# Performance work log

Measured on AMD Instinct MI355X. Metric: run time of the kernel, lower is better.

Reference implementation:

```python
import jax, jax.numpy as jnp
import numpy as np

B, T, C, H = 2, 2048, 1024, 16
HD = C // H  # 64

def setup_inputs() -> dict:
    key = jax.random.key(0)
    ks = jax.random.split(key, 9)
    s = 0.02
    return {
        "x": jax.random.normal(ks[0], (B, T, C), jnp.float32),
        "Wq": jax.random.normal(ks[1], (C, C), jnp.float32) * s,
        "bq": jax.random.normal(ks[2], (C,), jnp.float32) * s,
        "Wk": jax.random.normal(ks[3], (C, C), jnp.float32) * s,
        "bk": jax.random.normal(ks[4], (C,), jnp.float32) * s,
        "Wv": jax.random.normal(ks[5], (C, C), jnp.float32) * s,
        "bv": jax.random.normal(ks[6], (C,), jnp.float32) * s,
        "Wp": jax.random.normal(ks[7], (C, C), jnp.float32) * s,
        "bp": jax.random.normal(ks[8], (C,), jnp.float32) * s,
    }

def reference(x, Wq, bq, Wk, bk, Wv, bv, Wp, bp):
    Bb, Tt, Cc = x.shape
    hd = Cc // H
    # project and split heads: [B, H, T, hd]
    def heads(W, b):
        return (x @ W.T + b).reshape(Bb, Tt, H, hd).transpose(0, 2, 1, 3)
    q, k, v = heads(Wq, bq), heads(Wk, bk), heads(Wv, bv)
    scale = 1.0 / np.sqrt(hd).astype(np.float32)
    att = jnp.einsum('bhqd,bhkd->bhqk', q, k) * scale
    causal = jnp.tril(jnp.ones((Tt, Tt), bool))
    att = jnp.where(causal[None, None], att, -jnp.inf)
    att = jax.nn.softmax(att, axis=-1)
    y = jnp.einsum('bhqk,bhkd->bhqd', att, v)
    y = y.transpose(0, 2, 1, 3).reshape(Bb, Tt, Cc)
    return y @ Wp.T + bp
```

## Files before the change

kernel.cpp:

```cpp
#include <hip/hip_runtime.h>
#include <hip/hip_bf16.h>

#define Tsz 2048
#define Csz 1024
#define Hn 16

typedef short s8v __attribute__((ext_vector_type(8)));
typedef short s4v __attribute__((ext_vector_type(4)));
typedef float f4v __attribute__((ext_vector_type(4)));

#define QSCALE (0.125f * 1.44269504088896f)

__device__ __forceinline__ short bf_bits(float x) {
    __hip_bfloat16 t = __float2bfloat16(x);
    return *reinterpret_cast<short*>(&t);
}

__device__ __forceinline__ void gload_lds(const void* g, void* l) {
    __builtin_amdgcn_global_load_lds(
        (const __attribute__((address_space(1))) void*)g,
        (__attribute__((address_space(3))) void*)l, 16, 0, 0);
}

__global__ void cvt6(const float* __restrict__ x, const float* __restrict__ wq,
                     const float* __restrict__ wk, const float* __restrict__ wv,
                     const float* __restrict__ wp,
                     short* __restrict__ xo, short* __restrict__ qo,
                     short* __restrict__ ko, short* __restrict__ vo,
                     short* __restrict__ po) {
    const int bx = blockIdx.x;
    const float* in; short* out; int ib;
    if (bx < 4096) { in = x; out = xo; ib = bx; }
    else {
        const int r = bx - 4096, w = r >> 10;
        ib = r & 1023;
        switch (w) {
            case 0: in = wq; out = qo; break;
            case 1: in = wk; out = ko; break;
            case 2: in = wv; out = vo; break;
            default: in = wp; out = po; break;
        }
    }
    const int i = ib * 1024 + threadIdx.x * 4;
    float4 v = *(const float4*)(in + i);
    short4 o;
    o.x = bf_bits(v.x); o.y = bf_bits(v.y); o.z = bf_bits(v.z); o.w = bf_bits(v.w);
    *(short4*)(out + i) = o;
}

__global__ __launch_bounds__(256, 3) void qkv_gemm(
    const short* __restrict__ X,
    const short* __restrict__ Wq, const short* __restrict__ Wk, const short* __restrict__ Wv,
    const float* __restrict__ bq, const float* __restrict__ bk, const float* __restrict__ bv,
    short* __restrict__ Qo, short* __restrict__ Ko, short* __restrict__ Vto)
{
    const int z = blockIdx.z;
    const short* W = (z == 0) ? Wq : (z == 1) ? Wk : Wv;
    const float* bias = (z == 0) ? bq : (z == 1) ? bk : bv;

    __shared__ __align__(16) short Ash[128 * 32];
    __shared__ __align__(16) short Bsh[128 * 32];
    __shared__ __align__(16) short TR[64 * 72];

    const int tid = threadIdx.x, lane = tid & 63, wave = tid >> 6;
    const int ln = lane & 15, hi = lane >> 4;
    const int m0 = blockIdx.x * 128, n0 = blockIdx.y * 128;
    const int wm = (wave >> 1) * 64, wn = (wave & 1) * 64;

    const short* Ag = X + (size_t)(m0 + (tid >> 2)) * Csz + (tid & 3) * 8;
    const short* Bg = W + (size_t)(n0 + (tid >> 2)) * Csz + (tid & 3) * 8;

    f4v acc[4][4];
    #pragma unroll
    for (int mt = 0; mt < 4; mt++)
        #pragma unroll
        for (int nt = 0; nt < 4; nt++)
            #pragma unroll
            for (int i = 0; i < 4; i++) acc[mt][nt][i] = 0.f;

    for (int k0 = 0; k0 < Csz; k0 += 32) {
        __syncthreads();
        gload_lds(Ag + k0, Ash + tid * 8);
        gload_lds(Ag + k0 + (size_t)64 * Csz, Ash + 2048 + tid * 8);
        gload_lds(Bg + k0, Bsh + tid * 8);
        gload_lds(Bg + k0 + (size_t)64 * Csz, Bsh + 2048 + tid * 8);
        __syncthreads();

        s8v af[4], bfr[4];
        #pragma unroll
        for (int mt = 0; mt < 4; mt++)
            af[mt] = *(const s8v*)(Ash + (wm + mt * 16 + ln) * 32 + hi * 8);
        #pragma unroll
        for (int nt = 0; nt < 4; nt++)
            bfr[nt] = *(const s8v*)(Bsh + (wn + nt * 16 + ln) * 32 + hi * 8);
        #pragma unroll
        for (int mt = 0; mt < 4; mt++)
            #pragma unroll
            for (int nt = 0; nt < 4; nt++)
                acc[mt][nt] = __builtin_amdgcn_mfma_f32_16x16x32_bf16(af[mt], bfr[nt], acc[mt][nt], 0, 0, 0);
    }

    if (z == 2) {
        const int b = m0 >> 11, t0 = m0 & 2047;
        float bvv[4];
        #pragma unroll
        for (int nt = 0; nt < 4; nt++) bvv[nt] = bias[n0 + wn + nt * 16 + ln];
        #pragma unroll
        for (int ph = 0; ph < 4; ph++) {
            const int mh = ph >> 1, nh = ph & 1;
            __syncthreads();
            if ((wave >> 1) == mh && (wave & 1) == nh) {
                #pragma unroll
                for (int mt = 0; mt < 4; mt++)
                    #pragma unroll
                    for (int nt = 0; nt < 4; nt++) {
                        s4v pk;
                        #pragma unroll
                        for (int i = 0; i < 4; i++) pk[i] = bf_bits(acc[mt][nt][i] + bvv[nt]);
                        *(s4v*)(TR + (nt * 16 + ln) * 72 + mt * 16 + hi * 4) = pk;
                    }
            }
            __syncthreads();
            const int chl = tid >> 2, seg = tid & 3;
            const s8v r0 = *(const s8v*)(TR + chl * 72 + seg * 16);
            const s8v r1 = *(const s8v*)(TR + chl * 72 + seg * 16 + 8);
            short* dst = Vto + (size_t)(b * 1024 + n0 + nh * 64 + chl) * Tsz + t0 + mh * 64 + seg * 16;
            *(s8v*)(dst) = r0;
            *(s8v*)(dst + 8) = r1;
        }
        return;
    }

    const float scale = (z == 0) ? QSCALE : 1.0f;
    short* out = (z == 0) ? Qo : Ko;

    #pragma unroll
    for (int nt = 0; nt < 4; nt++) {
        const int col = n0 + wn + nt * 16 + ln;
        const float bvv = bias[col];
        #pragma unroll
        for (int mt = 0; mt < 4; mt++) {
            const int row0 = m0 + wm + mt * 16 + hi * 4;
            #pragma unroll
            for (int i = 0; i < 4; i++)
                out[(size_t)(row0 + i) * Csz + col] = bf_bits((acc[mt][nt][i] + bvv) * scale);
        }
    }
}

__global__ __launch_bounds__(256, 2) void proj_gemm(
    const short* __restrict__ A, const short* __restrict__ W,
    const float* __restrict__ bias, float* __restrict__ out)
{
    __shared__ __align__(16) short Ash[128 * 32];
    __shared__ __align__(16) short Bsh[128 * 32];

    const int tid = threadIdx.x, lane = tid & 63, wave = tid >> 6;
    const int ln = lane & 15, hi = lane >> 4;
    const int m0 = blockIdx.x * 128, n0 = blockIdx.y * 128;
    const int wm = (wave >> 1) * 64, wn = (wave & 1) * 64;

    const short* Ag = A + (size_t)(m0 + (tid >> 2)) * Csz + (tid & 3) * 8;
    const short* Bg = W + (size_t)(n0 + (tid >> 2)) * Csz + (tid & 3) * 8;

    f4v acc[4][4];
    #pragma unroll
    for (int mt = 0; mt < 4; mt++)
        #pragma unroll
        for (int nt = 0; nt < 4; nt++)
            #pragma unroll
            for (int i = 0; i < 4; i++) acc[mt][nt][i] = 0.f;

    for (int k0 = 0; k0 < Csz; k0 += 32) {
        __syncthreads();
        gload_lds(Ag + k0, Ash + tid * 8);
        gload_lds(Ag + k0 + (size_t)64 * Csz, Ash + 2048 + tid * 8);
        gload_lds(Bg + k0, Bsh + tid * 8);
        gload_lds(Bg + k0 + (size_t)64 * Csz, Bsh + 2048 + tid * 8);
        __syncthreads();

        s8v af[4], bfr[4];
        #pragma unroll
        for (int mt = 0; mt < 4; mt++)
            af[mt] = *(const s8v*)(Ash + (wm + mt * 16 + ln) * 32 + hi * 8);
        #pragma unroll
        for (int nt = 0; nt < 4; nt++)
            bfr[nt] = *(const s8v*)(Bsh + (wn + nt * 16 + ln) * 32 + hi * 8);
        #pragma unroll
        for (int mt = 0; mt < 4; mt++)
            #pragma unroll
            for (int nt = 0; nt < 4; nt++)
                acc[mt][nt] = __builtin_amdgcn_mfma_f32_16x16x32_bf16(af[mt], bfr[nt], acc[mt][nt], 0, 0, 0);
    }

    #pragma unroll
    for (int nt = 0; nt < 4; nt++) {
        const int col = n0 + wn + nt * 16 + ln;
        const float bvv = bias[col];
        #pragma unroll
        for (int mt = 0; mt < 4; mt++)
            #pragma unroll
            for (int i = 0; i < 4; i++)
                out[(size_t)(m0 + wm + mt * 16 + hi * 4 + i) * Csz + col] = acc[mt][nt][i] + bvv;
    }
}

__global__ __launch_bounds__(512, 2) void attn7(
    const short* __restrict__ Q, const short* __restrict__ Kg,
    const short* __restrict__ Vt, short* __restrict__ Y)
{
    __shared__ __align__(16) short Ksh[2][64 * 72];
    __shared__ __align__(16) short Vsh[2][64 * 72];
    __shared__ __align__(16) short Psh[8][16 * 72];

    const int tid = threadIdx.x, lane = tid & 63, wave = tid >> 6;
    const int wv = wave & 3, g = wave >> 2;
    const int ln = lane & 15, hi = lane >> 4;
    const int p = blockIdx.x;
    const int qts[2] = { g ? 15 - p : p, g ? 16 + p : 31 - p };
    const int bh = blockIdx.y;
    const size_t base = (size_t)(bh >> 4) * Tsz * Csz + (size_t)(bh & 15) * 64;
    const size_t vtbase = (size_t)bh * 64 * Tsz;
    const int qrel = wv * 16 + ln;
    short* Pq = Psh[wave];

    s8v qf[2][2];
    #pragma unroll
    for (int t = 0; t < 2; t++)
        #pragma unroll
        for (int kk = 0; kk < 2; kk++)
            qf[t][kk] = *(const s8v*)(Q + base + (size_t)(qts[t] * 64 + qrel) * Csz + kk * 32 + hi * 8);

    f4v o[2][4];
    float lsum[2] = {0.f, 0.f};
    #pragma unroll
    for (int t = 0; t < 2; t++)
        #pragma unroll
        for (int dt = 0; dt < 4; dt++)
            #pragma unroll
            for (int i = 0; i < 4; i++) o[t][dt][i] = 0.f;

    const int sr = tid >> 3, sc = (tid & 7) * 8;
    const short* Kp = Kg + base + (size_t)sr * Csz + sc;
    const short* Vp = Vt + vtbase + (size_t)sr * Tsz + sc;
    const int swo = sr * 72 + sc;

    const int nkb = 32 - p;

    s8v kR = *(const s8v*)(Kp);
    s8v vR = *(const s8v*)(Vp);
    *(s8v*)(&Ksh[0][swo]) = kR;
    *(s8v*)(&Vsh[0][swo]) = vR;
    kR = *(const s8v*)(Kp + (size_t)64 * Csz);
    vR = *(const s8v*)(Vp + 64);
    __syncthreads();

    for (int kb = 0; kb < nkb; kb++) {
        const int buf = kb & 1;
        if (kb + 1 < nkb) {
            *(s8v*)(&Ksh[buf ^ 1][swo]) = kR;
            *(s8v*)(&Vsh[buf ^ 1][swo]) = vR;
            const int knx = (kb + 2 < nkb) ? (kb + 2) * 64 : (nkb - 1) * 64;
            kR = *(const s8v*)(Kp + (size_t)knx * Csz);
            vR = *(const s8v*)(Vp + knx);
        }

        s8v kf[2][4], vf[2][4];
        #pragma unroll
        for (int nt = 0; nt < 4; nt++)
            #pragma unroll
            for (int kk = 0; kk < 2; kk++) {
                kf[kk][nt] = *(const s8v*)(&Ksh[buf][(nt * 16 + ln) * 72 + kk * 32 + hi * 8]);
                vf[kk][nt] = *(const s8v*)(&Vsh[buf][(nt * 16 + ln) * 72 + kk * 32 + hi * 8]);
            }

        #pragma unroll
        for (int t = 0; t < 2; t++) {
            if (kb > qts[t]) continue;
            const bool dg = (kb == qts[t]);

            f4v s[4];
            #pragma unroll
            for (int nt = 0; nt < 4; nt++) {
                #pragma unroll
                for (int i = 0; i < 4; i++) s[nt][i] = 0.f;
                s[nt] = __builtin_amdgcn_mfma_f32_16x16x32_bf16(kf[0][nt], qf[t][0], s[nt], 0, 0, 0);
                s[nt] = __builtin_amdgcn_mfma_f32_16x16x32_bf16(kf[1][nt], qf[t][1], s[nt], 0, 0, 0);
            }

            #pragma unroll
            for (int nt = 0; nt < 4; nt++) {
                float pv[4];
                #pragma unroll
                for (int i = 0; i < 4; i++) pv[i] = exp2f(s[nt][i]);
                if (dg) {
                    const int kr = nt * 16 + hi * 4;
                    #pragma unroll
                    for (int i = 0; i < 4; i++)
                        if (kr + i > qrel) pv[i] = 0.f;
                }
                lsum[t] += (pv[0] + pv[1]) + (pv[2] + pv[3]);
                s4v w;
                #pragma unroll
                for (int i = 0; i < 4; i++) w[i] = bf_bits(pv[i]);
                *(s4v*)(Pq + ln * 72 + nt * 16 + hi * 4) = w;
            }
            const s8v pb0 = *(const s8v*)(Pq + ln * 72 + hi * 8);
            const s8v pb1 = *(const s8v*)(Pq + ln * 72 + 32 + hi * 8);

            #pragma unroll
            for (int dt = 0; dt < 4; dt++) {
                o[t][dt] = __builtin_amdgcn_mfma_f32_16x16x32_bf16(vf[0][dt], pb0, o[t][dt], 0, 0, 0);
                o[t][dt] = __builtin_amdgcn_mfma_f32_16x16x32_bf16(vf[1][dt], pb1, o[t][dt], 0, 0, 0);
            }
        }
        __syncthreads();
    }

    #pragma unroll
    for (int t = 0; t < 2; t++) {
        float l = lsum[t];
        l += __shfl_xor(l, 16);
        l += __shfl_xor(l, 32);
        const float inv = 1.0f / l;
        const int qrow = qts[t] * 64 + qrel;
        #pragma unroll
        for (int dt = 0; dt < 4; dt++) {
            s4v w;
            #pragma unroll
            for (int i = 0; i < 4; i++) w[i] = bf_bits(o[t][dt][i] * inv);
            *(s4v*)(Y + base + (size_t)qrow * Csz + dt * 16 + hi * 4) = w;
        }
    }
}

extern "C" void kernel_launch(void* const* d_in, const int* in_sizes, int n_in,
                              void* d_out, int out_size, void* d_ws, size_t ws_size,
                              hipStream_t stream) {
    const float* x  = (const float*)d_in[0];
    const float* Wq = (const float*)d_in[1];
    const float* bq = (const float*)d_in[2];
    const float* Wk = (const float*)d_in[3];
    const float* bk = (const float*)d_in[4];
    const float* Wv = (const float*)d_in[5];
    const float* bv = (const float*)d_in[6];
    const float* Wp = (const float*)d_in[7];
    const float* bp = (const float*)d_in[8];

    char* ws = (char*)d_ws;
    short* Xb  = (short*)(ws);
    short* Wqb = (short*)(ws + (8u  << 20));
    short* Wkb = (short*)(ws + (10u << 20));
    short* Wvb = (short*)(ws + (12u << 20));
    short* Wpb = (short*)(ws + (14u << 20));
    short* Qb  = (short*)(ws + (16u << 20));
    short* Kb  = (short*)(ws + (24u << 20));
    short* Vtb = (short*)(ws + (32u << 20));
    short* Yb  = (short*)(ws + (40u << 20));

    hipLaunchKernelGGL(cvt6, dim3(8192), dim3(256), 0, stream,
                       x, Wq, Wk, Wv, Wp, Xb, Wqb, Wkb, Wvb, Wpb);

    hipLaunchKernelGGL(qkv_gemm, dim3(32, 8, 3), dim3(256), 0, stream,
                       Xb, Wqb, Wkb, Wvb, bq, bk, bv, Qb, Kb, Vtb);

    hipLaunchKernelGGL(attn7, dim3(8, 32), dim3(512), 0, stream, Qb, Kb, Vtb, Yb);

    hipLaunchKernelGGL(proj_gemm, dim3(32, 8), dim3(256), 0, stream, Yb, Wpb, bp, (float*)d_out);
}
```

Baseline: 191.4 us.

## Split attention into 256-thread blocks with 32 query rows per wave

Rewrites the attention kernel so each 256-thread block processes a balanced pair of query tiles, with each wave computing 32 query rows against shared K/V tiles. The grid doubles to 512 blocks to improve CU fill, and per-wave work per LDS fragment load increases. Waves whose query tile is finished skip fragment loads. In exchange, K/V tiles are reloaded by twice as many blocks, and the QKV GEMM occupancy hint is lowered to give it more registers.

```diff
diff --git a/kernel.cpp b/kernel.cpp
--- a/kernel.cpp
+++ b/kernel.cpp
@@ -48,7 +48,7 @@
     *(short4*)(out + i) = o;
 }
 
-__global__ __launch_bounds__(256, 3) void qkv_gemm(
+__global__ __launch_bounds__(256, 2) void qkv_gemm(
     const short* __restrict__ X,
     const short* __restrict__ Wq, const short* __restrict__ Wk, const short* __restrict__ Wv,
     const float* __restrict__ bq, const float* __restrict__ bk, const float* __restrict__ bv,
@@ -205,130 +205,146 @@
     }
 }
 
-__global__ __launch_bounds__(512, 2) void attn7(
+__global__ __launch_bounds__(256, 2) void attn8(
     const short* __restrict__ Q, const short* __restrict__ Kg,
     const short* __restrict__ Vt, short* __restrict__ Y)
 {
     __shared__ __align__(16) short Ksh[2][64 * 72];
     __shared__ __align__(16) short Vsh[2][64 * 72];
-    __shared__ __align__(16) short Psh[8][16 * 72];
+    __shared__ __align__(16) short Psh[4][32 * 72];
 
     const int tid = threadIdx.x, lane = tid & 63, wave = tid >> 6;
-    const int wv = wave & 3, g = wave >> 2;
     const int ln = lane & 15, hi = lane >> 4;
     const int p = blockIdx.x;
-    const int qts[2] = { g ? 15 - p : p, g ? 16 + p : 31 - p };
+    const int qt = (wave >> 1) ? (31 - p) : p;
+    const int qh = wave & 1;
+    const int q0 = qt * 64 + qh * 32;
     const int bh = blockIdx.y;
     const size_t base = (size_t)(bh >> 4) * Tsz * Csz + (size_t)(bh & 15) * 64;
     const size_t vtbase = (size_t)bh * 64 * Tsz;
-    const int qrel = wv * 16 + ln;
     short* Pq = Psh[wave];
 
     s8v qf[2][2];
     #pragma unroll
-    for (int t = 0; t < 2; t++)
+    for (int j = 0; j < 2; j++)
         #pragma unroll
         for (int kk = 0; kk < 2; kk++)
-            qf[t][kk] = *(const s8v*)(Q + base + (size_t)(qts[t] * 64 + qrel) * Csz + kk * 32 + hi * 8);
+            qf[j][kk] = *(const s8v*)(Q + base + (size_t)(q0 + j * 16 + ln) * Csz + kk * 32 + hi * 8);
 
     f4v o[2][4];
     float lsum[2] = {0.f, 0.f};
     #pragma unroll
-    for (int t = 0; t < 2; t++)
+    for (int j = 0; j < 2; j++)
         #pragma unroll
         for (int dt = 0; dt < 4; dt++)
             #pragma unroll
-            for (int i = 0; i < 4; i++) o[t][dt][i] = 0.f;
-
-    const int sr = tid >> 3, sc = (tid & 7) * 8;
+            for (int i = 0; i < 4; i++) o[j][dt][i] = 0.f;
+
+    const int sr = tid >> 2, sc = (tid & 3) * 16;
     const short* Kp = Kg + base + (size_t)sr * Csz + sc;
     const short* Vp = Vt + vtbase + (size_t)sr * Tsz + sc;
     const int swo = sr * 72 + sc;
 
     const int nkb = 32 - p;
 
-    s8v kR = *(const s8v*)(Kp);
-    s8v vR = *(const s8v*)(Vp);
-    *(s8v*)(&Ksh[0][swo]) = kR;
-    *(s8v*)(&Vsh[0][swo]) = vR;
-    kR = *(const s8v*)(Kp + (size_t)64 * Csz);
-    vR = *(const s8v*)(Vp + 64);
+    s8v kR0 = *(const s8v*)(Kp);
+    s8v kR1 = *(const s8v*)(Kp + 8);
+    s8v vR0 = *(const s8v*)(Vp);
+    s8v vR1 = *(const s8v*)(Vp + 8);
+    *(s8v*)(&Ksh[0][swo]) = kR0; *(s8v*)(&Ksh[0][swo + 8]) = kR1;
+    *(s8v*)(&Vsh[0][swo]) = vR0; *(s8v*)(&Vsh[0][swo + 8]) = vR1;
+    kR0 = *(const s8v*)(Kp + (size_t)64 * Csz);
+    kR1 = *(const s8v*)(Kp + (size_t)64 * Csz + 8);
+    vR0 = *(const s8v*)(Vp + 64);
+    vR1 = *(const s8v*)(Vp + 64 + 8);
     __syncthreads();
 
     for (int kb = 0; kb < nkb; kb++) {
         const int buf = kb & 1;
         if (kb + 1 < nkb) {
-            *(s8v*)(&Ksh[buf ^ 1][swo]) = kR;
-            *(s8v*)(&Vsh[buf ^ 1][swo]) = vR;
+            *(s8v*)(&Ksh[buf ^ 1][swo]) = kR0; *(s8v*)(&Ksh[buf ^ 1][swo + 8]) = kR1;
+            *(s8v*)(&Vsh[buf ^ 1][swo]) = vR0; *(s8v*)(&Vsh[buf ^ 1][swo + 8]) = vR1;
             const int knx = (kb + 2 < nkb) ? (kb + 2) * 64 : (nkb - 1) * 64;
-            kR = *(const s8v*)(Kp + (size_t)knx * Csz);
-            vR = *(const s8v*)(Vp + knx);
-        }
-
-        s8v kf[2][4], vf[2][4];
-        #pragma unroll
-        for (int nt = 0; nt < 4; nt++)
-            #pragma unroll
-            for (int kk = 0; kk < 2; kk++) {
-                kf[kk][nt] = *(const s8v*)(&Ksh[buf][(nt * 16 + ln) * 72 + kk * 32 + hi * 8]);
-                vf[kk][nt] = *(const s8v*)(&Vsh[buf][(nt * 16 + ln) * 72 + kk * 32 + hi * 8]);
-            }
-
-        #pragma unroll
-        for (int t = 0; t < 2; t++) {
-            if (kb > qts[t]) continue;
-            const bool dg = (kb == qts[t]);
-
-            f4v s[4];
-            #pragma unroll
-            for (int nt = 0; nt < 4; nt++) {
-                #pragma unroll
-                for (int i = 0; i < 4; i++) s[nt][i] = 0.f;
-                s[nt] = __builtin_amdgcn_mfma_f32_16x16x32_bf16(kf[0][nt], qf[t][0], s[nt], 0, 0, 0);
-                s[nt] = __builtin_amdgcn_mfma_f32_16x16x32_bf16(kf[1][nt], qf[t][1], s[nt], 0, 0, 0);
-            }
-
-            #pragma unroll
-            for (int nt = 0; nt < 4; nt++) {
-                float pv[4];
-                #pragma unroll
-                for (int i = 0; i < 4; i++) pv[i] = exp2f(s[nt][i]);
-                if (dg) {
-                    const int kr = nt * 16 + hi * 4;
+            kR0 = *(const s8v*)(Kp + (size_t)knx * Csz);
+            kR1 = *(const s8v*)(Kp + (size_t)knx * Csz + 8);
+            vR0 = *(const s8v*)(Vp + knx);
+            vR1 = *(const s8v*)(Vp + knx + 8);
+        }
+
+        if (kb <= qt) {
+            s8v kf[2][4], vf[2][4];
+            #pragma unroll
+            for (int nt = 0; nt < 4; nt++)
+                #pragma unroll
+                for (int kk = 0; kk < 2; kk++) {
+                    kf[kk][nt] = *(const s8v*)(&Ksh[buf][(nt * 16 + ln) * 72 + kk * 32 + hi * 8]);
+                    vf[kk][nt] = *(const s8v*)(&Vsh[buf][(nt * 16 + ln) * 72 + kk * 32 + hi * 8]);
+                }
+
+            const bool dg = (kb == qt);
+
+            f4v s[4][2];
+            #pragma unroll
+            for (int nt = 0; nt < 4; nt++)
+                #pragma unroll
+                for (int j = 0; j < 2; j++) {
                     #pragma unroll
-                    for (int i = 0; i < 4; i++)
-                        if (kr + i > qrel) pv[i] = 0.f;
+                    for (int i = 0; i < 4; i++) s[nt][j][i] = 0.f;
+                    s[nt][j] = __builtin_amdgcn_mfma_f32_16x16x32_bf16(kf[0][nt], qf[j][0], s[nt][j], 0, 0, 0);
+                    s[nt][j] = __builtin_amdgcn_mfma_f32_16x16x32_bf16(kf[1][nt], qf[j][1], s[nt][j], 0, 0, 0);
                 }
-                lsum[t] += (pv[0] + pv[1]) + (pv[2] + pv[3]);
-                s4v w;
-                #pragma unroll
-                for (int i = 0; i < 4; i++) w[i] = bf_bits(pv[i]);
-                *(s4v*)(Pq + ln * 72 + nt * 16 + hi * 4) = w;
-            }
-            const s8v pb0 = *(const s8v*)(Pq + ln * 72 + hi * 8);
-            const s8v pb1 = *(const s8v*)(Pq + ln * 72 + 32 + hi * 8);
-
-            #pragma unroll
-            for (int dt = 0; dt < 4; dt++) {
-                o[t][dt] = __builtin_amdgcn_mfma_f32_16x16x32_bf16(vf[0][dt], pb0, o[t][dt], 0, 0, 0);
-                o[t][dt] = __builtin_amdgcn_mfma_f32_16x16x32_bf16(vf[1][dt], pb1, o[t][dt], 0, 0, 0);
-            }
-        }
-        __syncthreads();
-    }
-
-    #pragma unroll
-    for (int t = 0; t < 2; t++) {
-        float l = lsum[t];
+
+            #pragma unroll
+            for (int nt = 0; nt < 4; nt++)
+                #pragma unroll
+                for (int j = 0; j < 2; j++) {
+                    float pv[4];
+                    #pragma unroll
+                    for (int i = 0; i < 4; i++) pv[i] = exp2f(s[nt][j][i]);
+                    if (dg) {
+                        const int kr = nt * 16 + hi * 4;
+                        const int qr = qh * 32 + j * 16 + ln;
+                        #pragma unroll
+                        for (int i = 0; i < 4; i++)
+                            if (kr + i > qr) pv[i] = 0.f;
+                    }
+                    lsum[j] += (pv[0] + pv[1]) + (pv[2] + pv[3]);
+                    s4v w;
+                    #pragma unroll
+                    for (int i = 0; i < 4; i++) w[i] = bf_bits(pv[i]);
+                    *(s4v*)(Pq + (j * 16 + ln) * 72 + nt * 16 + hi * 4) = w;
+                }
+
+            s8v pb[2][2];
+            #pragma unroll
+            for (int j = 0; j < 2; j++)
+                #pragma unroll
+                for (int kk = 0; kk < 2; kk++)
+                    pb[j][kk] = *(const s8v*)(Pq + (j * 16 + ln) * 72 + kk * 32 + hi * 8);
+
+            #pragma unroll
+            for (int dt = 0; dt < 4; dt++)
+                #pragma unroll
+                for (int j = 0; j < 2; j++) {
+                    o[j][dt] = __builtin_amdgcn_mfma_f32_16x16x32_bf16(vf[0][dt], pb[j][0], o[j][dt], 0, 0, 0);
+                    o[j][dt] = __builtin_amdgcn_mfma_f32_16x16x32_bf16(vf[1][dt], pb[j][1], o[j][dt], 0, 0, 0);
+                }
+        }
+        __syncthreads();
+    }
+
+    #pragma unroll
+    for (int j = 0; j < 2; j++) {
+        float l = lsum[j];
         l += __shfl_xor(l, 16);
         l += __shfl_xor(l, 32);
         const float inv = 1.0f / l;
-        const int qrow = qts[t] * 64 + qrel;
+        const int qrow = q0 + j * 16 + ln;
         #pragma unroll
         for (int dt = 0; dt < 4; dt++) {
             s4v w;
             #pragma unroll
-            for (int i = 0; i < 4; i++) w[i] = bf_bits(o[t][dt][i] * inv);
+            for (int i = 0; i < 4; i++) w[i] = bf_bits(o[j][dt][i] * inv);
             *(s4v*)(Y + base + (size_t)qrow * Csz + dt * 16 + hi * 4) = w;
         }
     }
@@ -364,7 +380,7 @@
     hipLaunchKernelGGL(qkv_gemm, dim3(32, 8, 3), dim3(256), 0, stream,
                        Xb, Wqb, Wkb, Wvb, bq, bk, bv, Qb, Kb, Vtb);
 
-    hipLaunchKernelGGL(attn7, dim3(8, 32), dim3(512), 0, stream, Qb, Kb, Vtb, Yb);
+    hipLaunchKernelGGL(attn8, dim3(16, 32), dim3(256), 0, stream, Qb, Kb, Vtb, Yb);
 
     hipLaunchKernelGGL(proj_gemm, dim3(32, 8), dim3(256), 0, stream, Yb, Wpb, bp, (float*)d_out);
 }
```

After: 204.7 us. +6.9%, slower.
